# Kernel optimization log

Hardware: AMD Instinct MI355X
Metric: run time of the kernel (lower is better)

The kernel has to match this reference:

```python
import jax, jax.numpy as jnp
import numpy as np

E = 512   # embed_size
H = 8     # attn_heads
B = 4
S = 1024
EPS = 1e-5


def setup_inputs() -> dict:
    key = jax.random.key(0)
    ks = jax.random.split(key, 12)
    s_in = 1.0 / np.sqrt(E)
    s_cat = 1.0 / np.sqrt(H * E)
    s_ff = 1.0 / np.sqrt(4 * E)
    return {
        "x": jax.random.normal(ks[0], (B, S, E), jnp.float32),
        # projection weights stored [in, out] (transpose of torch Linear.weight)
        "Wq": jax.random.uniform(ks[1], (E, H * E), jnp.float32, -s_in, s_in),
        "Wk": jax.random.uniform(ks[2], (E, H * E), jnp.float32, -s_in, s_in),
        "Wv": jax.random.uniform(ks[3], (E, H * E), jnp.float32, -s_in, s_in),
        "Wo": jax.random.uniform(ks[4], (H * E, E), jnp.float32, -s_cat, s_cat),
        "g1": jnp.ones((E,), jnp.float32),
        "b1": jnp.zeros((E,), jnp.float32),
        "g2": jnp.ones((E,), jnp.float32),
        "b2": jnp.zeros((E,), jnp.float32),
        "W1": jax.random.uniform(ks[5], (E, 4 * E), jnp.float32, -s_in, s_in),
        "c1": jax.random.uniform(ks[6], (4 * E,), jnp.float32, -s_in, s_in),
        "W2": jax.random.uniform(ks[7], (4 * E, E), jnp.float32, -s_ff, s_ff),
        "c2": jax.random.uniform(ks[8], (E,), jnp.float32, -s_ff, s_ff),
    }


def _layernorm(x, g, b):
    mu = jnp.mean(x, axis=-1, keepdims=True)
    var = jnp.var(x, axis=-1, keepdims=True)
    return (x - mu) * jax.lax.rsqrt(var + EPS) * g + b


def reference(x, Wq, Wk, Wv, Wo, g1, b1, g2, b2, W1, c1, W2, c2):
    Bsz, Sl, Es = x.shape
    # project to [B, S, H, E] per-head (head dim == embed_size in this module)
    q = (x @ Wq).reshape(Bsz, Sl, H, Es)
    k = (x @ Wk).reshape(Bsz, Sl, H, Es)
    v = (x @ Wv).reshape(Bsz, Sl, H, Es)
    # scaled dot-product attention; note scale uses sqrt(embed_size)
    scores = jnp.einsum("bqhd,bkhd->bhqk", q, k) / jnp.sqrt(jnp.float32(Es))
    attn = jax.nn.softmax(scores, axis=-1)
    out = jnp.einsum("bhqk,bkhd->bqhd", attn, v).reshape(Bsz, Sl, H * Es)
    attn_scores = out @ Wo
    normed = _layernorm(attn_scores + x, g1, b1)
    h = jax.nn.relu(normed @ W1 + c1)
    ff = h @ W2 + c2
    return _layernorm(ff + normed, g2, b2)
```

## Files before the change

kernel.cpp:

```cpp
#include <hip/hip_runtime.h>
#include <hip/hip_fp8.h>

#define EBD   512
#define NHEAD 8
#define BSZ   4
#define SEQ   1024
#define MTOK  4096
#define HE    4096
#define FFD   2048

typedef __bf16 bf16;
typedef __attribute__((ext_vector_type(8))) __bf16 bf16x8;
typedef __attribute__((ext_vector_type(4))) float  f32x4;
typedef __attribute__((ext_vector_type(8))) int    i32x8;

__device__ __forceinline__ void async_load16(const void* g, void* l) {
  __builtin_amdgcn_global_load_lds(
      (const __attribute__((address_space(1))) void*)g,
      (__attribute__((address_space(3))) void*)l, 16, 0, 0);
}

#if __has_builtin(__builtin_amdgcn_cvt_pk_fp8_f32)
__device__ __forceinline__ int pk_fp8_lo(float a, float b, int old) {
  return __builtin_amdgcn_cvt_pk_fp8_f32(a, b, old, false);
}
__device__ __forceinline__ int pk_fp8_hi(float a, float b, int old) {
  return __builtin_amdgcn_cvt_pk_fp8_f32(a, b, old, true);
}
#else
__device__ __forceinline__ int pk_fp8_lo(float a, float b, int old) {
  __hip_fp8_e4m3 fa(a), fb(b);
  int w = (int)fa.__x | ((int)fb.__x << 8);
  return (old & ~0xffff) | w;
}
__device__ __forceinline__ int pk_fp8_hi(float a, float b, int old) {
  __hip_fp8_e4m3 fa(a), fb(b);
  int w = (int)fa.__x | ((int)fb.__x << 8);
  return (old & 0xffff) | (w << 16);
}
#endif

#if __has_builtin(__builtin_amdgcn_cvt_f32_fp8)
#define F8DEC(v, k) __builtin_amdgcn_cvt_f32_fp8((v), (k))
#else
__device__ __forceinline__ float __f8dec_sw(int v, int k) {
  __hip_fp8_e4m3 f; f.__x = (unsigned char)((v >> (8 * k)) & 0xff); return (float)f;
}
#define F8DEC(v, k) __f8dec_sw((v), (k))
#endif

__device__ __forceinline__ int4 pack16_fp8(const float* v) {
  int4 r;
  r.x = pk_fp8_hi(v[2],  v[3],  pk_fp8_lo(v[0],  v[1],  0));
  r.y = pk_fp8_hi(v[6],  v[7],  pk_fp8_lo(v[4],  v[5],  0));
  r.z = pk_fp8_hi(v[10], v[11], pk_fp8_lo(v[8],  v[9],  0));
  r.w = pk_fp8_hi(v[14], v[15], pk_fp8_lo(v[12], v[13], 0));
  return r;
}

__global__ void gemm_bt(const bf16* __restrict__ A, const bf16* __restrict__ Bt,
                        float* __restrict__ outF, bf16* __restrict__ outB,
                        const float* __restrict__ bias, const float* __restrict__ res,
                        int lda, int ldb, int ldc, int ldr, int K,
                        long long bAb, long long bAh, long long bBb, long long bBh,
                        long long bCb, long long bCh, int zdiv,
                        float scale, int relu)
{
  __shared__ __attribute__((aligned(16))) float Smem[4 * 2304];
  bf16* As = (bf16*)Smem;
  bf16* Bs = (bf16*)Smem + 128 * 64;

  const int t = threadIdx.x;
  const int w = t >> 6, l = t & 63;
  const int m0 = blockIdx.y * 128, n0 = blockIdx.x * 128;
  const int z = blockIdx.z;
  const int zb = z / zdiv, zh = z - zb * zdiv;

  const bf16* Ab = A + (size_t)zb * bAb + (size_t)zh * bAh;
  const bf16* Bb = Bt + (size_t)zb * bBb + (size_t)zh * bBh;

  const int srow = t >> 3;
  const int gch  = (((t & 7) ^ ((t >> 4) & 7))) * 8;
  const bf16* pA = Ab + (size_t)(m0 + srow) * lda + gch;
  const bf16* pB = Bb + (size_t)(n0 + srow) * ldb + gch;
  const size_t ldA32 = (size_t)32 * lda;
  const size_t ldB32 = (size_t)32 * ldb;

  bf16* ldsA = As + w * 512;
  bf16* ldsB = Bs + w * 512;

  const int wm = (w >> 1) * 64, wn = (w & 1) * 64;
  const int lr = l & 15;
  const int lc = l >> 4;

  f32x4 acc[4][4];
#pragma unroll
  for (int i = 0; i < 4; ++i)
#pragma unroll
    for (int j = 0; j < 4; ++j) { f32x4 zv = {0.f, 0.f, 0.f, 0.f}; acc[i][j] = zv; }

  const int nkt = K >> 6;
  for (int kt = 0; kt < nkt; ++kt) {
    __syncthreads();
#pragma unroll
    for (int j = 0; j < 4; ++j) {
      async_load16(pA + j * ldA32, ldsA + j * 2048);
      async_load16(pB + j * ldB32, ldsB + j * 2048);
    }
    pA += 64; pB += 64;
    __syncthreads();
#pragma unroll
    for (int ks = 0; ks < 2; ++ks) {
      bf16x8 af[4], bv[4];
#pragma unroll
      for (int i = 0; i < 4; ++i) {
        const int row = wm + i * 16 + lr;
        const int p = (ks * 4 + lc) ^ ((row >> 1) & 7);
        af[i] = *(const bf16x8*)&As[row * 64 + p * 8];
      }
#pragma unroll
      for (int i = 0; i < 4; ++i) {
        const int row = wn + i * 16 + lr;
        const int p = (ks * 4 + lc) ^ ((row >> 1) & 7);
        bv[i] = *(const bf16x8*)&Bs[row * 64 + p * 8];
      }
#pragma unroll
      for (int mi = 0; mi < 4; ++mi)
#pragma unroll
        for (int ni = 0; ni < 4; ++ni)
          acc[mi][ni] = __builtin_amdgcn_mfma_f32_16x16x32_bf16(af[mi], bv[ni], acc[mi][ni], 0, 0, 0);
    }
  }

  float* cs = Smem + w * 2304;
  const size_t offC = (size_t)zb * bCb + (size_t)zh * bCh;
  const int rq = (l >> 4) * 4;

#pragma unroll
  for (int p = 0; p < 2; ++p) {
    __syncthreads();
#pragma unroll
    for (int ni2 = 0; ni2 < 2; ++ni2) {
      const int ni = 2 * p + ni2;
      const int cl = ni2 * 16 + lr;
#pragma unroll
      for (int mi = 0; mi < 4; ++mi)
#pragma unroll
        for (int r = 0; r < 4; ++r)
          cs[(mi * 16 + rq + r) * 36 + cl] = acc[mi][ni][r];
    }
    __syncthreads();
    if (outB) {
      const int rl0 = l >> 2, c8 = (l & 3) * 8;
#pragma unroll
      for (int sub = 0; sub < 4; ++sub) {
        const int rl = sub * 16 + rl0;
        const int rowg = m0 + wm + rl;
        const int colg = n0 + wn + p * 32 + c8;
        float vv[8];
        *(f32x4*)&vv[0] = *(const f32x4*)&cs[rl * 36 + c8];
        *(f32x4*)&vv[4] = *(const f32x4*)&cs[rl * 36 + c8 + 4];
#pragma unroll
        for (int j = 0; j < 8; ++j) vv[j] *= scale;
        if (bias) {
          const float4 b0 = *(const float4*)(bias + colg);
          const float4 b1 = *(const float4*)(bias + colg + 4);
          vv[0] += b0.x; vv[1] += b0.y; vv[2] += b0.z; vv[3] += b0.w;
          vv[4] += b1.x; vv[5] += b1.y; vv[6] += b1.z; vv[7] += b1.w;
        }
        if (res) {
          const float4 r0 = *(const float4*)(res + (size_t)rowg * ldr + colg);
          const float4 r1 = *(const float4*)(res + (size_t)rowg * ldr + colg + 4);
          vv[0] += r0.x; vv[1] += r0.y; vv[2] += r0.z; vv[3] += r0.w;
          vv[4] += r1.x; vv[5] += r1.y; vv[6] += r1.z; vv[7] += r1.w;
        }
        if (relu)
#pragma unroll
          for (int j = 0; j < 8; ++j) vv[j] = fmaxf(vv[j], 0.0f);
        union { bf16 h8[8]; float4 f; } u;
#pragma unroll
        for (int j = 0; j < 8; ++j) u.h8[j] = (bf16)vv[j];
        *(float4*)(outB + offC + (size_t)rowg * ldc + colg) = u.f;
      }
    } else {
      const int rl0 = l >> 3, c4 = (l & 7) * 4;
#pragma unroll
      for (int sub = 0; sub < 8; ++sub) {
        const int rl = sub * 8 + rl0;
        const int rowg = m0 + wm + rl;
        const int colg = n0 + wn + p * 32 + c4;
        float4 v = *(const float4*)&cs[rl * 36 + c4];
        v.x *= scale; v.y *= scale; v.z *= scale; v.w *= scale;
        *(float4*)(outF + offC + (size_t)rowg * ldc + colg) = v;
      }
    }
  }
}

__global__ void gemm_f8(const unsigned char* __restrict__ A, const unsigned char* __restrict__ Bt,
                        float* __restrict__ outF, unsigned char* __restrict__ out8,
                        unsigned char* __restrict__ vTout, const float* __restrict__ rowdiv,
                        int lda, int ldb, int ldc, int K,
                        long long bAb, long long bAh, long long bBb, long long bBh,
                        long long bCb, long long bCh, int zdiv,
                        float scale, int mode, int vmode)
{
  __shared__ __attribute__((aligned(16))) float Smem[4 * 2304];
  unsigned char* As = (unsigned char*)Smem;
  unsigned char* Bs = As + 128 * 128;

  const int t = threadIdx.x;
  const int w = t >> 6, l = t & 63;
  const int m0 = blockIdx.y * 128, n0 = blockIdx.x * 128;
  const int z = blockIdx.z;
  const int zb = z / zdiv, zh = z - zb * zdiv;

  const unsigned char* Ab = A + (size_t)zb * bAb + (size_t)zh * bAh;
  const unsigned char* Bb = Bt + (size_t)zb * bBb + (size_t)zh * bBh;

  const int srow = t >> 3;
  const int gch  = ((t & 7) ^ ((t >> 4) & 7)) * 16;
  const unsigned char* pA = Ab + (size_t)(m0 + srow) * lda + gch;
  const unsigned char* pB = Bb + (size_t)(n0 + srow) * ldb + gch;
  const size_t ldA32 = (size_t)32 * lda;
  const size_t ldB32 = (size_t)32 * ldb;

  unsigned char* ldsA = As + w * 1024;
  unsigned char* ldsB = Bs + w * 1024;

  const int wm = (w >> 1) * 64, wn = (w & 1) * 64;
  const int lr = l & 15;
  const int lg = l >> 4;

  f32x4 acc[4][4];
#pragma unroll
  for (int i = 0; i < 4; ++i)
#pragma unroll
    for (int j = 0; j < 4; ++j) { f32x4 zv = {0.f, 0.f, 0.f, 0.f}; acc[i][j] = zv; }

  const int nkt = K >> 7;
  for (int kt = 0; kt < nkt; ++kt) {
    __syncthreads();
#pragma unroll
    for (int j = 0; j < 4; ++j) {
      async_load16(pA + j * ldA32, ldsA + j * 4096);
      async_load16(pB + j * ldB32, ldsB + j * 4096);
    }
    pA += 128; pB += 128;
    __syncthreads();
    i32x8 bv[4];
#pragma unroll
    for (int i = 0; i < 4; ++i) {
      const int row = wn + i * 16 + lr;
      const int s = (row >> 1) & 7;
      const int c0 = (2 * lg) ^ s, c1 = (2 * lg + 1) ^ s;
      const int4 lo = *(const int4*)&Bs[row * 128 + c0 * 16];
      const int4 hi = *(const int4*)&Bs[row * 128 + c1 * 16];
      i32x8 v = {lo.x, lo.y, lo.z, lo.w, hi.x, hi.y, hi.z, hi.w};
      bv[i] = v;
    }
#pragma unroll
    for (int mi = 0; mi < 4; ++mi) {
      const int row = wm + mi * 16 + lr;
      const int s = (row >> 1) & 7;
      const int c0 = (2 * lg) ^ s, c1 = (2 * lg + 1) ^ s;
      const int4 lo = *(const int4*)&As[row * 128 + c0 * 16];
      const int4 hi = *(const int4*)&As[row * 128 + c1 * 16];
      i32x8 af = {lo.x, lo.y, lo.z, lo.w, hi.x, hi.y, hi.z, hi.w};
#pragma unroll
      for (int ni = 0; ni < 4; ++ni)
        acc[mi][ni] = __builtin_amdgcn_mfma_scale_f32_16x16x128_f8f6f4(
            af, bv[ni], acc[mi][ni], 0, 0, 0, 0x7f7f7f7f, 0, 0x7f7f7f7f);
    }
  }

  float* cs = Smem + w * 2304;
  const size_t offC = (size_t)zb * bCb + (size_t)zh * bCh;
  const int rq = (l >> 4) * 4;

  if (vmode && n0 >= 8192) {
    const int b8 = (m0 + wm) >> 10;
    const int s0 = (m0 + wm) & 1023;
#pragma unroll
    for (int ph = 0; ph < 2; ++ph) {
      __syncthreads();
#pragma unroll
      for (int ni2 = 0; ni2 < 2; ++ni2) {
        const int ni = 2 * ph + ni2;
        const int cl = ni2 * 16 + lr;
#pragma unroll
        for (int mi = 0; mi < 4; ++mi)
#pragma unroll
          for (int r = 0; r < 4; ++r)
            cs[cl * 68 + mi * 16 + rq + r] = acc[mi][ni][r];
      }
      __syncthreads();
      const int c = l & 31, half = l >> 5;
      int e = (n0 - 8192) + wn + ph * 32 + c;
      const int h = e >> 9; e &= 511;
      unsigned char* dst = vTout + (((size_t)(b8 * 8 + h) * 512 + e) << 10) + s0 + half * 32;
      float vv[32];
#pragma unroll
      for (int j = 0; j < 8; ++j)
        *(f32x4*)&vv[4 * j] = *(const f32x4*)&cs[c * 68 + half * 32 + 4 * j];
#pragma unroll
      for (int j = 0; j < 32; ++j) vv[j] *= scale;
      *(int4*)dst        = pack16_fp8(&vv[0]);
      *(int4*)(dst + 16) = pack16_fp8(&vv[16]);
    }
    return;
  }

#pragma unroll
  for (int ph = 0; ph < 2; ++ph) {
    __syncthreads();
#pragma unroll
    for (int ni2 = 0; ni2 < 2; ++ni2) {
      const int ni = 2 * ph + ni2;
      const int cl = ni2 * 16 + lr;
#pragma unroll
      for (int mi = 0; mi < 4; ++mi)
#pragma unroll
        for (int r = 0; r < 4; ++r)
          cs[(mi * 16 + rq + r) * 36 + cl] = acc[mi][ni][r];
    }
    __syncthreads();
    if (mode == 3) {
      const int rl0 = l >> 3, c4 = (l & 7) * 4;
#pragma unroll
      for (int sub = 0; sub < 8; ++sub) {
        const int rl = sub * 8 + rl0;
        const int rowg = m0 + wm + rl;
        const int colg = n0 + wn + ph * 32 + c4;
        float4 v = *(const float4*)&cs[rl * 36 + c4];
        v.x *= scale; v.y *= scale; v.z *= scale; v.w *= scale;
        *(float4*)(outF + offC + (size_t)rowg * ldc + colg) = v;
      }
    } else {
      const int rl0 = l >> 1, c16 = (l & 1) * 16;
#pragma unroll
      for (int sub = 0; sub < 2; ++sub) {
        const int rl = sub * 32 + rl0;
        const int rowg = m0 + wm + rl;
        const int colg = n0 + wn + ph * 32 + c16;
        float vv[16];
#pragma unroll
        for (int j2 = 0; j2 < 4; ++j2)
          *(f32x4*)&vv[4 * j2] = *(const f32x4*)&cs[rl * 36 + c16 + 4 * j2];
        if (mode == 1) {
#pragma unroll
          for (int j = 0; j < 16; ++j) vv[j] = __expf(vv[j] * scale);
        } else if (mode == 2) {
          const float d = scale / rowdiv[(size_t)z * SEQ + rowg];
#pragma unroll
          for (int j = 0; j < 16; ++j) vv[j] *= d;
        } else {
#pragma unroll
          for (int j = 0; j < 16; ++j) vv[j] *= scale;
        }
        *(int4*)(out8 + offC + (size_t)rowg * ldc + colg) = pack16_fp8(vv);
      }
    }
  }
}

__global__ void cast_x_f8(const float* __restrict__ in, unsigned char* __restrict__ out, int n16) {
  int i = blockIdx.x * 256 + threadIdx.x;
  if (i >= n16) return;
  const float4* p = (const float4*)in + (size_t)i * 4;
  float vv[16];
  *(f32x4*)&vv[0]  = *(const f32x4*)&p[0];
  *(f32x4*)&vv[4]  = *(const f32x4*)&p[1];
  *(f32x4*)&vv[8]  = *(const f32x4*)&p[2];
  *(f32x4*)&vv[12] = *(const f32x4*)&p[3];
  ((int4*)out)[i] = pack16_fp8(vv);
}

struct WTList {
  const float* in[6];
  void* out[6];
  float scale[6];
  int isf8[6];
  int K[6], N[6];
  int start[7];
};
__global__ void transpose_cast_all(WTList L) {
  __shared__ float tile[32][33];
  int bid = blockIdx.x;
  int i = 0;
  while (bid >= L.start[i + 1]) ++i;
  int rel = bid - L.start[i];
  const int N = L.N[i], K = L.K[i];
  const int nx = N >> 5;
  const int n0 = (rel % nx) * 32, k0 = (rel / nx) * 32;
  const float* in = L.in[i];
  const float sc = L.scale[i];
  int tx = threadIdx.x, ty = threadIdx.y;
#pragma unroll
  for (int j = 0; j < 32; j += 8)
    tile[ty + j][tx] = in[(size_t)(k0 + ty + j) * N + n0 + tx];
  __syncthreads();
  if (L.isf8[i]) {
    unsigned char* out = (unsigned char*)L.out[i];
#pragma unroll
    for (int j = 0; j < 32; j += 8)
      out[(size_t)(n0 + ty + j) * K + k0 + tx] =
          (unsigned char)(pk_fp8_lo(tile[tx][ty + j] * sc, 0.f, 0) & 0xff);
  } else {
    bf16* out = (bf16*)L.out[i];
#pragma unroll
    for (int j = 0; j < 32; j += 8)
      out[(size_t)(n0 + ty + j) * K + k0 + tx] = (bf16)(tile[tx][ty + j] * sc);
  }
}

__global__ void rowsum_f8(const unsigned char* __restrict__ e, float* __restrict__ lsum) {
  int ln = threadIdx.x & 63, w = threadIdx.x >> 6;
  size_t row = (size_t)blockIdx.x * 4 + w;
  const int4 v = ((const int4*)(e + row * SEQ))[ln];
  float s = 0.0f;
  s += F8DEC(v.x, 0) + F8DEC(v.x, 1) + F8DEC(v.x, 2) + F8DEC(v.x, 3);
  s += F8DEC(v.y, 0) + F8DEC(v.y, 1) + F8DEC(v.y, 2) + F8DEC(v.y, 3);
  s += F8DEC(v.z, 0) + F8DEC(v.z, 1) + F8DEC(v.z, 2) + F8DEC(v.z, 3);
  s += F8DEC(v.w, 0) + F8DEC(v.w, 1) + F8DEC(v.w, 2) + F8DEC(v.w, 3);
#pragma unroll
  for (int d = 1; d < 64; d <<= 1) s += __shfl_xor(s, d);
  if (ln == 0) lsum[row] = s;
}

__global__ void reduce_ln(const float* __restrict__ parts, int ns,
                          const float* __restrict__ res, const float* __restrict__ bias,
                          const float* __restrict__ gw, const float* __restrict__ bw,
                          float* __restrict__ outF, bf16* __restrict__ outB) {
  int l = threadIdx.x & 63, w = threadIdx.x >> 6;
  int row = blockIdx.x * 4 + w;
  const long long pstr = (long long)MTOK * EBD;
  float4 a = {0.f, 0.f, 0.f, 0.f}, b = {0.f, 0.f, 0.f, 0.f};
  for (int s = 0; s < ns; ++s) {
    const float4* p = (const float4*)(parts + s * pstr + (size_t)row * EBD);
    float4 pa = p[l], pb = p[l + 64];
    a.x += pa.x; a.y += pa.y; a.z += pa.z; a.w += pa.w;
    b.x += pb.x; b.y += pb.y; b.z += pb.z; b.w += pb.w;
  }
  {
    const float4* p = (const float4*)(res + (size_t)row * EBD);
    float4 pa = p[l], pb = p[l + 64];
    a.x += pa.x; a.y += pa.y; a.z += pa.z; a.w += pa.w;
    b.x += pb.x; b.y += pb.y; b.z += pb.z; b.w += pb.w;
  }
  if (bias) {
    const float4* p = (const float4*)bias;
    float4 pa = p[l], pb = p[l + 64];
    a.x += pa.x; a.y += pa.y; a.z += pa.z; a.w += pa.w;
    b.x += pb.x; b.y += pb.y; b.z += pb.z; b.w += pb.w;
  }
  float s = a.x + a.y + a.z + a.w + b.x + b.y + b.z + b.w;
  float q = a.x * a.x + a.y * a.y + a.z * a.z + a.w * a.w
          + b.x * b.x + b.y * b.y + b.z * b.z + b.w * b.w;
#pragma unroll
  for (int d = 1; d < 64; d <<= 1) { s += __shfl_xor(s, d); q += __shfl_xor(q, d); }
  float mu = s * (1.0f / EBD);
  float var = q * (1.0f / EBD) - mu * mu;
  float rs = rsqrtf(var + 1e-5f);
  const float4* g4 = (const float4*)gw;
  const float4* b4 = (const float4*)bw;
  float4 ga = g4[l], gb = g4[l + 64], ba = b4[l], bb = b4[l + 64];
  float4 o0, o1;
  o0.x = (a.x - mu) * rs * ga.x + ba.x;
  o0.y = (a.y - mu) * rs * ga.y + ba.y;
  o0.z = (a.z - mu) * rs * ga.z + ba.z;
  o0.w = (a.w - mu) * rs * ga.w + ba.w;
  o1.x = (b.x - mu) * rs * gb.x + bb.x;
  o1.y = (b.y - mu) * rs * gb.y + bb.y;
  o1.z = (b.z - mu) * rs * gb.z + bb.z;
  o1.w = (b.w - mu) * rs * gb.w + bb.w;
  if (outF) {
    float4* q4 = (float4*)(outF + (size_t)row * EBD);
    q4[l] = o0; q4[l + 64] = o1;
  }
  if (outB) {
    union { bf16 h[4]; float2 f; } u0, u1;
    u0.h[0] = (bf16)o0.x; u0.h[1] = (bf16)o0.y; u0.h[2] = (bf16)o0.z; u0.h[3] = (bf16)o0.w;
    u1.h[0] = (bf16)o1.x; u1.h[1] = (bf16)o1.y; u1.h[2] = (bf16)o1.z; u1.h[3] = (bf16)o1.w;
    float2* r2 = (float2*)(outB + (size_t)row * EBD);
    r2[l] = u0.f; r2[l + 64] = u1.f;
  }
}

extern "C" void kernel_launch(void* const* d_in, const int* in_sizes, int n_in,
                              void* d_out, int out_size, void* d_ws, size_t ws_size,
                              hipStream_t stream) {
  const float* x  = (const float*)d_in[0];
  const float* Wq = (const float*)d_in[1];
  const float* Wk = (const float*)d_in[2];
  const float* Wv = (const float*)d_in[3];
  const float* Wo = (const float*)d_in[4];
  const float* g1 = (const float*)d_in[5];
  const float* b1 = (const float*)d_in[6];
  const float* g2 = (const float*)d_in[7];
  const float* b2 = (const float*)d_in[8];
  const float* W1 = (const float*)d_in[9];
  const float* c1 = (const float*)d_in[10];
  const float* W2 = (const float*)d_in[11];
  const float* c2 = (const float*)d_in[12];
  float* out = (float*)d_out;

  char* p = (char*)d_ws;
  auto take = [&](size_t bytes) { char* r = p; p += (bytes + 255) & ~(size_t)255; return r; };
  unsigned char* xb8    = (unsigned char*)take((size_t)MTOK * EBD);
  unsigned char* qk8    = (unsigned char*)take((size_t)MTOK * 2 * HE);
  unsigned char* vT8    = (unsigned char*)take((size_t)32 * EBD * SEQ);
  unsigned char* sc8    = (unsigned char*)take((size_t)32 * SEQ * SEQ);
  float*         lsum   = (float*)        take((size_t)32 * SEQ * 4);
  unsigned char* ao8    = (unsigned char*)take((size_t)MTOK * HE);
  float*         nF     = (float*)        take((size_t)MTOK * EBD * 4);
  bf16*          nB     = (bf16*)         take((size_t)MTOK * EBD * 2);
  bf16*          hb     = (bf16*)         take((size_t)MTOK * FFD * 2);
  unsigned char* Wqkv8T = (unsigned char*)take((size_t)3 * HE * EBD);
  unsigned char* Wo8T   = (unsigned char*)take((size_t)EBD * HE);
  bf16*          W1T    = (bf16*)         take((size_t)FFD * EBD * 2);
  bf16*          W2T    = (bf16*)         take((size_t)EBD * FFD * 2);
  float* parts = (float*)sc8;

  auto gemmf8 = [&](const unsigned char* A, const unsigned char* Bt, float* oF,
                    unsigned char* o8, unsigned char* vTo, const float* rdiv,
                    int Mm, int Nn, int Kk, int lda_, int ldb_, int ldc_,
                    long long bAb, long long bAh, long long bBb, long long bBh,
                    long long bCb, long long bCh, int zdiv_, int batch,
                    float sc_, int mode_, int vmode_) {
    dim3 g(Nn / 128, Mm / 128, batch);
    gemm_f8<<<g, dim3(256), 0, stream>>>(A, Bt, oF, o8, vTo, rdiv, lda_, ldb_, ldc_, Kk,
        bAb, bAh, bBb, bBh, bCb, bCh, zdiv_, sc_, mode_, vmode_);
  };
  auto gemmbf = [&](const bf16* A, const bf16* Bt, float* oF, bf16* oB,
                    const float* bias, const float* res,
                    int Mm, int Nn, int Kk, int lda_, int ldb_, int ldc_, int ldr_,
                    long long bAh, long long bBh, long long bCh, int batch,
                    float sc_, int relu_) {
    dim3 g(Nn / 128, Mm / 128, batch);
    gemm_bt<<<g, dim3(256), 0, stream>>>(A, Bt, oF, oB, bias, res,
        lda_, ldb_, ldc_, ldr_, Kk, 0, bAh, 0, bBh, 0, bCh, 64, sc_, relu_);
  };

  cast_x_f8<<<dim3(MTOK * EBD / 16 / 256), dim3(256), 0, stream>>>(x, xb8, MTOK * EBD / 16);
  {
    WTList L;
    const float* ins[6] = {Wq, Wk, Wv, Wo, W1, W2};
    void* outs[6] = {Wqkv8T, Wqkv8T + (size_t)HE * EBD, Wqkv8T + (size_t)2 * HE * EBD,
                     Wo8T, W1T, W2T};
    float scs[6] = {8.f, 8.f, 8.f, 16.f, 1.f, 1.f};
    int f8s[6] = {1, 1, 1, 1, 0, 0};
    int Ks[6] = {EBD, EBD, EBD, HE, EBD, FFD};
    int Ns[6] = {HE, HE, HE, EBD, FFD, EBD};
    int acc = 0;
    for (int i = 0; i < 6; ++i) {
      L.in[i] = ins[i]; L.out[i] = outs[i]; L.scale[i] = scs[i]; L.isf8[i] = f8s[i];
      L.K[i] = Ks[i]; L.N[i] = Ns[i]; L.start[i] = acc;
      acc += (Ks[i] / 32) * (Ns[i] / 32);
    }
    L.start[6] = acc;
    transpose_cast_all<<<dim3(acc), dim3(32, 8), 0, stream>>>(L);
  }

  gemmf8(xb8, Wqkv8T, nullptr, qk8, vT8, nullptr, MTOK, 3 * HE, EBD,
         EBD, EBD, 2 * HE, 0, 0, 0, 0, 0, 0, 64, 1, 0.125f, 0, 1);

  const float qs = 0.04419417382415922f;
  gemmf8(qk8, qk8 + HE, nullptr, sc8, nullptr, nullptr, SEQ, SEQ, EBD,
         2 * HE, 2 * HE, SEQ,
         (long long)SEQ * 2 * HE, EBD, (long long)SEQ * 2 * HE, EBD,
         (long long)8 * SEQ * SEQ, (long long)SEQ * SEQ, 8, 32, qs, 1, 0);

  rowsum_f8<<<dim3(32 * SEQ / 4), dim3(256), 0, stream>>>(sc8, lsum);

  gemmf8(sc8, vT8, nullptr, ao8, nullptr, lsum, SEQ, EBD, SEQ,
         SEQ, SEQ, HE,
         (long long)8 * SEQ * SEQ, (long long)SEQ * SEQ,
         (long long)8 * EBD * SEQ, (long long)EBD * SEQ,
         (long long)SEQ * HE, (long long)EBD, 8, 32, 16.0f, 2, 0);

  gemmf8(ao8, Wo8T, parts, nullptr, nullptr, nullptr, MTOK, EBD, 1024,
         HE, HE, EBD, 0, 1024, 0, 1024, 0, (long long)MTOK * EBD, 64, 4,
         1.0f / 256.0f, 3, 0);
  reduce_ln<<<dim3(MTOK / 4), dim3(256), 0, stream>>>(parts, 4, x, nullptr, g1, b1, nF, nB);

  gemmbf(nB, W1T, nullptr, hb, c1, nullptr, MTOK, FFD, EBD,
         EBD, EBD, FFD, 0, 0, 0, 0, 1, 1.0f, 1);
  gemmbf(hb, W2T, parts, nullptr, nullptr, nullptr, MTOK, EBD, 512,
         FFD, FFD, EBD, 0, 512, 512, (long long)MTOK * EBD, 4, 1.0f, 0);
  reduce_ln<<<dim3(MTOK / 4), dim3(256), 0, stream>>>(parts, 4, nF, c2, g2, b2, out, nullptr);
}
```

Measured before the change: 296.9 us.

## Move FFN GEMMs to FP8 and fuse softmax row sums into score GEMM

The two feed-forward GEMMs now use the FP8 GEMM kernel instead of the bf16 one. W1 and W2 are pre-scaled and cast to FP8, and the LayerNorm output and hidden activations are stored as FP8, with bias and ReLU moved into the FP8 epilogue. The separate rowsum kernel is dropped: the score GEMM accumulates exp row sums with atomics into lsum, which cast_x_f8 zeroes in one extra block. This removes a kernel launch, a full reread of the score matrix, and bf16 traffic and MFMA cost in the FFN, in exchange for lower FFN precision and float atomics whose summation order is nondeterministic.

After: 278.9 us. 6.1% less time.

```diff
diff --git a/kernel.cpp b/kernel.cpp
--- a/kernel.cpp
+++ b/kernel.cpp
@@ -10,7 +10,6 @@
 #define FFD   2048
 
 typedef __bf16 bf16;
-typedef __attribute__((ext_vector_type(8))) __bf16 bf16x8;
 typedef __attribute__((ext_vector_type(4))) float  f32x4;
 typedef __attribute__((ext_vector_type(8))) int    i32x8;
 
@@ -38,15 +37,6 @@
   int w = (int)fa.__x | ((int)fb.__x << 8);
   return (old & 0xffff) | (w << 16);
 }
-#endif
-
-#if __has_builtin(__builtin_amdgcn_cvt_f32_fp8)
-#define F8DEC(v, k) __builtin_amdgcn_cvt_f32_fp8((v), (k))
-#else
-__device__ __forceinline__ float __f8dec_sw(int v, int k) {
-  __hip_fp8_e4m3 f; f.__x = (unsigned char)((v >> (8 * k)) & 0xff); return (float)f;
-}
-#define F8DEC(v, k) __f8dec_sw((v), (k))
 #endif
 
 __device__ __forceinline__ int4 pack16_fp8(const float* v) {
@@ -58,152 +48,14 @@
   return r;
 }
 
-__global__ void gemm_bt(const bf16* __restrict__ A, const bf16* __restrict__ Bt,
-                        float* __restrict__ outF, bf16* __restrict__ outB,
-                        const float* __restrict__ bias, const float* __restrict__ res,
-                        int lda, int ldb, int ldc, int ldr, int K,
-                        long long bAb, long long bAh, long long bBb, long long bBh,
-                        long long bCb, long long bCh, int zdiv,
-                        float scale, int relu)
-{
-  __shared__ __attribute__((aligned(16))) float Smem[4 * 2304];
-  bf16* As = (bf16*)Smem;
-  bf16* Bs = (bf16*)Smem + 128 * 64;
-
-  const int t = threadIdx.x;
-  const int w = t >> 6, l = t & 63;
-  const int m0 = blockIdx.y * 128, n0 = blockIdx.x * 128;
-  const int z = blockIdx.z;
-  const int zb = z / zdiv, zh = z - zb * zdiv;
-
-  const bf16* Ab = A + (size_t)zb * bAb + (size_t)zh * bAh;
-  const bf16* Bb = Bt + (size_t)zb * bBb + (size_t)zh * bBh;
-
-  const int srow = t >> 3;
-  const int gch  = (((t & 7) ^ ((t >> 4) & 7))) * 8;
-  const bf16* pA = Ab + (size_t)(m0 + srow) * lda + gch;
-  const bf16* pB = Bb + (size_t)(n0 + srow) * ldb + gch;
-  const size_t ldA32 = (size_t)32 * lda;
-  const size_t ldB32 = (size_t)32 * ldb;
-
-  bf16* ldsA = As + w * 512;
-  bf16* ldsB = Bs + w * 512;
-
-  const int wm = (w >> 1) * 64, wn = (w & 1) * 64;
-  const int lr = l & 15;
-  const int lc = l >> 4;
-
-  f32x4 acc[4][4];
-#pragma unroll
-  for (int i = 0; i < 4; ++i)
-#pragma unroll
-    for (int j = 0; j < 4; ++j) { f32x4 zv = {0.f, 0.f, 0.f, 0.f}; acc[i][j] = zv; }
-
-  const int nkt = K >> 6;
-  for (int kt = 0; kt < nkt; ++kt) {
-    __syncthreads();
-#pragma unroll
-    for (int j = 0; j < 4; ++j) {
-      async_load16(pA + j * ldA32, ldsA + j * 2048);
-      async_load16(pB + j * ldB32, ldsB + j * 2048);
-    }
-    pA += 64; pB += 64;
-    __syncthreads();
-#pragma unroll
-    for (int ks = 0; ks < 2; ++ks) {
-      bf16x8 af[4], bv[4];
-#pragma unroll
-      for (int i = 0; i < 4; ++i) {
-        const int row = wm + i * 16 + lr;
-        const int p = (ks * 4 + lc) ^ ((row >> 1) & 7);
-        af[i] = *(const bf16x8*)&As[row * 64 + p * 8];
-      }
-#pragma unroll
-      for (int i = 0; i < 4; ++i) {
-        const int row = wn + i * 16 + lr;
-        const int p = (ks * 4 + lc) ^ ((row >> 1) & 7);
-        bv[i] = *(const bf16x8*)&Bs[row * 64 + p * 8];
-      }
-#pragma unroll
-      for (int mi = 0; mi < 4; ++mi)
-#pragma unroll
-        for (int ni = 0; ni < 4; ++ni)
-          acc[mi][ni] = __builtin_amdgcn_mfma_f32_16x16x32_bf16(af[mi], bv[ni], acc[mi][ni], 0, 0, 0);
-    }
-  }
-
-  float* cs = Smem + w * 2304;
-  const size_t offC = (size_t)zb * bCb + (size_t)zh * bCh;
-  const int rq = (l >> 4) * 4;
-
-#pragma unroll
-  for (int p = 0; p < 2; ++p) {
-    __syncthreads();
-#pragma unroll
-    for (int ni2 = 0; ni2 < 2; ++ni2) {
-      const int ni = 2 * p + ni2;
-      const int cl = ni2 * 16 + lr;
-#pragma unroll
-      for (int mi = 0; mi < 4; ++mi)
-#pragma unroll
-        for (int r = 0; r < 4; ++r)
-          cs[(mi * 16 + rq + r) * 36 + cl] = acc[mi][ni][r];
-    }
-    __syncthreads();
-    if (outB) {
-      const int rl0 = l >> 2, c8 = (l & 3) * 8;
-#pragma unroll
-      for (int sub = 0; sub < 4; ++sub) {
-        const int rl = sub * 16 + rl0;
-        const int rowg = m0 + wm + rl;
-        const int colg = n0 + wn + p * 32 + c8;
-        float vv[8];
-        *(f32x4*)&vv[0] = *(const f32x4*)&cs[rl * 36 + c8];
-        *(f32x4*)&vv[4] = *(const f32x4*)&cs[rl * 36 + c8 + 4];
-#pragma unroll
-        for (int j = 0; j < 8; ++j) vv[j] *= scale;
-        if (bias) {
-          const float4 b0 = *(const float4*)(bias + colg);
-          const float4 b1 = *(const float4*)(bias + colg + 4);
-          vv[0] += b0.x; vv[1] += b0.y; vv[2] += b0.z; vv[3] += b0.w;
-          vv[4] += b1.x; vv[5] += b1.y; vv[6] += b1.z; vv[7] += b1.w;
-        }
-        if (res) {
-          const float4 r0 = *(const float4*)(res + (size_t)rowg * ldr + colg);
-          const float4 r1 = *(const float4*)(res + (size_t)rowg * ldr + colg + 4);
-          vv[0] += r0.x; vv[1] += r0.y; vv[2] += r0.z; vv[3] += r0.w;
-          vv[4] += r1.x; vv[5] += r1.y; vv[6] += r1.z; vv[7] += r1.w;
-        }
-        if (relu)
-#pragma unroll
-          for (int j = 0; j < 8; ++j) vv[j] = fmaxf(vv[j], 0.0f);
-        union { bf16 h8[8]; float4 f; } u;
-#pragma unroll
-        for (int j = 0; j < 8; ++j) u.h8[j] = (bf16)vv[j];
-        *(float4*)(outB + offC + (size_t)rowg * ldc + colg) = u.f;
-      }
-    } else {
-      const int rl0 = l >> 3, c4 = (l & 7) * 4;
-#pragma unroll
-      for (int sub = 0; sub < 8; ++sub) {
-        const int rl = sub * 8 + rl0;
-        const int rowg = m0 + wm + rl;
-        const int colg = n0 + wn + p * 32 + c4;
-        float4 v = *(const float4*)&cs[rl * 36 + c4];
-        v.x *= scale; v.y *= scale; v.z *= scale; v.w *= scale;
-        *(float4*)(outF + offC + (size_t)rowg * ldc + colg) = v;
-      }
-    }
-  }
-}
-
 __global__ void gemm_f8(const unsigned char* __restrict__ A, const unsigned char* __restrict__ Bt,
                         float* __restrict__ outF, unsigned char* __restrict__ out8,
                         unsigned char* __restrict__ vTout, const float* __restrict__ rowdiv,
+                        const float* __restrict__ bias, float* __restrict__ lsum,
                         int lda, int ldb, int ldc, int K,
                         long long bAb, long long bAh, long long bBb, long long bBh,
                         long long bCb, long long bCh, int zdiv,
-                        float scale, int mode, int vmode)
+                        float scale, int mode, int relu, int vmode)
 {
   __shared__ __attribute__((aligned(16))) float Smem[4 * 2304];
   unsigned char* As = (unsigned char*)Smem;
@@ -311,6 +163,9 @@
     return;
   }
 
+  const int rl0 = l >> 1, c16 = (l & 1) * 16;
+  float rsum[2] = {0.f, 0.f};
+
 #pragma unroll
   for (int ph = 0; ph < 2; ++ph) {
     __syncthreads();
@@ -326,10 +181,10 @@
     }
     __syncthreads();
     if (mode == 3) {
-      const int rl0 = l >> 3, c4 = (l & 7) * 4;
+      const int prl0 = l >> 3, c4 = (l & 7) * 4;
 #pragma unroll
       for (int sub = 0; sub < 8; ++sub) {
-        const int rl = sub * 8 + rl0;
+        const int rl = sub * 8 + prl0;
         const int rowg = m0 + wm + rl;
         const int colg = n0 + wn + ph * 32 + c4;
         float4 v = *(const float4*)&cs[rl * 36 + c4];
@@ -337,7 +192,6 @@
         *(float4*)(outF + offC + (size_t)rowg * ldc + colg) = v;
       }
     } else {
-      const int rl0 = l >> 1, c16 = (l & 1) * 16;
 #pragma unroll
       for (int sub = 0; sub < 2; ++sub) {
         const int rl = sub * 32 + rl0;
@@ -347,26 +201,57 @@
 #pragma unroll
         for (int j2 = 0; j2 < 4; ++j2)
           *(f32x4*)&vv[4 * j2] = *(const f32x4*)&cs[rl * 36 + c16 + 4 * j2];
+#pragma unroll
+        for (int j = 0; j < 16; ++j) vv[j] *= scale;
+        if (bias) {
+#pragma unroll
+          for (int j2 = 0; j2 < 4; ++j2) {
+            const float4 b0 = *(const float4*)(bias + colg + 4 * j2);
+            vv[4 * j2] += b0.x; vv[4 * j2 + 1] += b0.y;
+            vv[4 * j2 + 2] += b0.z; vv[4 * j2 + 3] += b0.w;
+          }
+        }
+        if (relu)
+#pragma unroll
+          for (int j = 0; j < 16; ++j) vv[j] = fmaxf(vv[j], 0.0f);
         if (mode == 1) {
-#pragma unroll
-          for (int j = 0; j < 16; ++j) vv[j] = __expf(vv[j] * scale);
+          float s = 0.0f;
+#pragma unroll
+          for (int j = 0; j < 16; ++j) { vv[j] = __expf(vv[j]); s += vv[j]; }
+          rsum[sub] += s;
         } else if (mode == 2) {
-          const float d = scale / rowdiv[(size_t)z * SEQ + rowg];
+          const float d = 1.0f / rowdiv[(size_t)z * SEQ + rowg];
 #pragma unroll
           for (int j = 0; j < 16; ++j) vv[j] *= d;
-        } else {
-#pragma unroll
-          for (int j = 0; j < 16; ++j) vv[j] *= scale;
         }
         *(int4*)(out8 + offC + (size_t)rowg * ldc + colg) = pack16_fp8(vv);
       }
     }
   }
-}
-
-__global__ void cast_x_f8(const float* __restrict__ in, unsigned char* __restrict__ out, int n16) {
+  if (mode == 1 && lsum) {
+#pragma unroll
+    for (int sub = 0; sub < 2; ++sub) {
+      float s = rsum[sub] + __shfl_xor(rsum[sub], 1);
+      if (!(l & 1)) {
+        const int rowg = m0 + wm + sub * 32 + rl0;
+        atomicAdd(&lsum[(size_t)z * SEQ + rowg], s);
+      }
+    }
+  }
+}
+
+__global__ void cast_x_f8(const float* __restrict__ in, unsigned char* __restrict__ out,
+                          int n16, float* __restrict__ lsum) {
   int i = blockIdx.x * 256 + threadIdx.x;
-  if (i >= n16) return;
+  if (i >= n16) {
+    if (blockIdx.x == (unsigned)(n16 / 256)) {
+      float4 zv = {0.f, 0.f, 0.f, 0.f};
+      float4* q = (float4*)lsum;
+#pragma unroll
+      for (int j = 0; j < 32; ++j) q[threadIdx.x * 32 + j] = zv;
+    }
+    return;
+  }
   const float4* p = (const float4*)in + (size_t)i * 4;
   float vv[16];
   *(f32x4*)&vv[0]  = *(const f32x4*)&p[0];
@@ -378,9 +263,8 @@
 
 struct WTList {
   const float* in[6];
-  void* out[6];
+  unsigned char* out[6];
   float scale[6];
-  int isf8[6];
   int K[6], N[6];
   int start[7];
 };
@@ -395,43 +279,22 @@
   const int n0 = (rel % nx) * 32, k0 = (rel / nx) * 32;
   const float* in = L.in[i];
   const float sc = L.scale[i];
+  unsigned char* out = L.out[i];
   int tx = threadIdx.x, ty = threadIdx.y;
 #pragma unroll
   for (int j = 0; j < 32; j += 8)
     tile[ty + j][tx] = in[(size_t)(k0 + ty + j) * N + n0 + tx];
   __syncthreads();
-  if (L.isf8[i]) {
-    unsigned char* out = (unsigned char*)L.out[i];
-#pragma unroll
-    for (int j = 0; j < 32; j += 8)
-      out[(size_t)(n0 + ty + j) * K + k0 + tx] =
-          (unsigned char)(pk_fp8_lo(tile[tx][ty + j] * sc, 0.f, 0) & 0xff);
-  } else {
-    bf16* out = (bf16*)L.out[i];
-#pragma unroll
-    for (int j = 0; j < 32; j += 8)
-      out[(size_t)(n0 + ty + j) * K + k0 + tx] = (bf16)(tile[tx][ty + j] * sc);
-  }
-}
-
-__global__ void rowsum_f8(const unsigned char* __restrict__ e, float* __restrict__ lsum) {
-  int ln = threadIdx.x & 63, w = threadIdx.x >> 6;
-  size_t row = (size_t)blockIdx.x * 4 + w;
-  const int4 v = ((const int4*)(e + row * SEQ))[ln];
-  float s = 0.0f;
-  s += F8DEC(v.x, 0) + F8DEC(v.x, 1) + F8DEC(v.x, 2) + F8DEC(v.x, 3);
-  s += F8DEC(v.y, 0) + F8DEC(v.y, 1) + F8DEC(v.y, 2) + F8DEC(v.y, 3);
-  s += F8DEC(v.z, 0) + F8DEC(v.z, 1) + F8DEC(v.z, 2) + F8DEC(v.z, 3);
-  s += F8DEC(v.w, 0) + F8DEC(v.w, 1) + F8DEC(v.w, 2) + F8DEC(v.w, 3);
-#pragma unroll
-  for (int d = 1; d < 64; d <<= 1) s += __shfl_xor(s, d);
-  if (ln == 0) lsum[row] = s;
+#pragma unroll
+  for (int j = 0; j < 32; j += 8)
+    out[(size_t)(n0 + ty + j) * K + k0 + tx] =
+        (unsigned char)(pk_fp8_lo(tile[tx][ty + j] * sc, 0.f, 0) & 0xff);
 }
 
 __global__ void reduce_ln(const float* __restrict__ parts, int ns,
                           const float* __restrict__ res, const float* __restrict__ bias,
                           const float* __restrict__ gw, const float* __restrict__ bw,
-                          float* __restrict__ outF, bf16* __restrict__ outB) {
+                          float* __restrict__ outF, unsigned char* __restrict__ out8) {
   int l = threadIdx.x & 63, w = threadIdx.x >> 6;
   int row = blockIdx.x * 4 + w;
   const long long pstr = (long long)MTOK * EBD;
@@ -478,12 +341,10 @@
     float4* q4 = (float4*)(outF + (size_t)row * EBD);
     q4[l] = o0; q4[l + 64] = o1;
   }
-  if (outB) {
-    union { bf16 h[4]; float2 f; } u0, u1;
-    u0.h[0] = (bf16)o0.x; u0.h[1] = (bf16)o0.y; u0.h[2] = (bf16)o0.z; u0.h[3] = (bf16)o0.w;
-    u1.h[0] = (bf16)o1.x; u1.h[1] = (bf16)o1.y; u1.h[2] = (bf16)o1.z; u1.h[3] = (bf16)o1.w;
-    float2* r2 = (float2*)(outB + (size_t)row * EBD);
-    r2[l] = u0.f; r2[l + 64] = u1.f;
+  if (out8) {
+    int* o = (int*)(out8 + (size_t)row * EBD);
+    o[l]      = pk_fp8_hi(o0.z, o0.w, pk_fp8_lo(o0.x, o0.y, 0));
+    o[l + 64] = pk_fp8_hi(o1.z, o1.w, pk_fp8_lo(o1.x, o1.y, 0));
   }
 }
 
@@ -514,47 +375,39 @@
   float*         lsum   = (float*)        take((size_t)32 * SEQ * 4);
   unsigned char* ao8    = (unsigned char*)take((size_t)MTOK * HE);
   float*         nF     = (float*)        take((size_t)MTOK * EBD * 4);
-  bf16*          nB     = (bf16*)         take((size_t)MTOK * EBD * 2);
-  bf16*          hb     = (bf16*)         take((size_t)MTOK * FFD * 2);
+  unsigned char* n8     = (unsigned char*)take((size_t)MTOK * EBD);
+  unsigned char* h8     = (unsigned char*)take((size_t)MTOK * FFD);
   unsigned char* Wqkv8T = (unsigned char*)take((size_t)3 * HE * EBD);
   unsigned char* Wo8T   = (unsigned char*)take((size_t)EBD * HE);
-  bf16*          W1T    = (bf16*)         take((size_t)FFD * EBD * 2);
-  bf16*          W2T    = (bf16*)         take((size_t)EBD * FFD * 2);
+  unsigned char* W18T   = (unsigned char*)take((size_t)FFD * EBD);
+  unsigned char* W28T   = (unsigned char*)take((size_t)EBD * FFD);
   float* parts = (float*)sc8;
 
   auto gemmf8 = [&](const unsigned char* A, const unsigned char* Bt, float* oF,
                     unsigned char* o8, unsigned char* vTo, const float* rdiv,
+                    const float* bias_, float* lsum_,
                     int Mm, int Nn, int Kk, int lda_, int ldb_, int ldc_,
                     long long bAb, long long bAh, long long bBb, long long bBh,
                     long long bCb, long long bCh, int zdiv_, int batch,
-                    float sc_, int mode_, int vmode_) {
+                    float sc_, int mode_, int relu_, int vmode_) {
     dim3 g(Nn / 128, Mm / 128, batch);
-    gemm_f8<<<g, dim3(256), 0, stream>>>(A, Bt, oF, o8, vTo, rdiv, lda_, ldb_, ldc_, Kk,
-        bAb, bAh, bBb, bBh, bCb, bCh, zdiv_, sc_, mode_, vmode_);
+    gemm_f8<<<g, dim3(256), 0, stream>>>(A, Bt, oF, o8, vTo, rdiv, bias_, lsum_,
+        lda_, ldb_, ldc_, Kk, bAb, bAh, bBb, bBh, bCb, bCh, zdiv_, sc_, mode_, relu_, vmode_);
   };
-  auto gemmbf = [&](const bf16* A, const bf16* Bt, float* oF, bf16* oB,
-                    const float* bias, const float* res,
-                    int Mm, int Nn, int Kk, int lda_, int ldb_, int ldc_, int ldr_,
-                    long long bAh, long long bBh, long long bCh, int batch,
-                    float sc_, int relu_) {
-    dim3 g(Nn / 128, Mm / 128, batch);
-    gemm_bt<<<g, dim3(256), 0, stream>>>(A, Bt, oF, oB, bias, res,
-        lda_, ldb_, ldc_, ldr_, Kk, 0, bAh, 0, bBh, 0, bCh, 64, sc_, relu_);
-  };
-
-  cast_x_f8<<<dim3(MTOK * EBD / 16 / 256), dim3(256), 0, stream>>>(x, xb8, MTOK * EBD / 16);
+
+  cast_x_f8<<<dim3(MTOK * EBD / 16 / 256 + 1), dim3(256), 0, stream>>>(
+      x, xb8, MTOK * EBD / 16, lsum);
   {
     WTList L;
     const float* ins[6] = {Wq, Wk, Wv, Wo, W1, W2};
-    void* outs[6] = {Wqkv8T, Wqkv8T + (size_t)HE * EBD, Wqkv8T + (size_t)2 * HE * EBD,
-                     Wo8T, W1T, W2T};
-    float scs[6] = {8.f, 8.f, 8.f, 16.f, 1.f, 1.f};
-    int f8s[6] = {1, 1, 1, 1, 0, 0};
+    unsigned char* outs[6] = {Wqkv8T, Wqkv8T + (size_t)HE * EBD, Wqkv8T + (size_t)2 * HE * EBD,
+                              Wo8T, W18T, W28T};
+    float scs[6] = {8.f, 8.f, 8.f, 16.f, 8.f, 16.f};
     int Ks[6] = {EBD, EBD, EBD, HE, EBD, FFD};
     int Ns[6] = {HE, HE, HE, EBD, FFD, EBD};
     int acc = 0;
     for (int i = 0; i < 6; ++i) {
-      L.in[i] = ins[i]; L.out[i] = outs[i]; L.scale[i] = scs[i]; L.isf8[i] = f8s[i];
+      L.in[i] = ins[i]; L.out[i] = outs[i]; L.scale[i] = scs[i];
       L.K[i] = Ks[i]; L.N[i] = Ns[i]; L.start[i] = acc;
       acc += (Ks[i] / 32) * (Ns[i] / 32);
     }
@@ -562,31 +415,33 @@
     transpose_cast_all<<<dim3(acc), dim3(32, 8), 0, stream>>>(L);
   }
 
-  gemmf8(xb8, Wqkv8T, nullptr, qk8, vT8, nullptr, MTOK, 3 * HE, EBD,
-         EBD, EBD, 2 * HE, 0, 0, 0, 0, 0, 0, 64, 1, 0.125f, 0, 1);
+  gemmf8(xb8, Wqkv8T, nullptr, qk8, vT8, nullptr, nullptr, nullptr,
+         MTOK, 3 * HE, EBD, EBD, EBD, 2 * HE,
+         0, 0, 0, 0, 0, 0, 64, 1, 0.125f, 0, 0, 1);
 
   const float qs = 0.04419417382415922f;
-  gemmf8(qk8, qk8 + HE, nullptr, sc8, nullptr, nullptr, SEQ, SEQ, EBD,
-         2 * HE, 2 * HE, SEQ,
+  gemmf8(qk8, qk8 + HE, nullptr, sc8, nullptr, nullptr, nullptr, lsum,
+         SEQ, SEQ, EBD, 2 * HE, 2 * HE, SEQ,
          (long long)SEQ * 2 * HE, EBD, (long long)SEQ * 2 * HE, EBD,
-         (long long)8 * SEQ * SEQ, (long long)SEQ * SEQ, 8, 32, qs, 1, 0);
-
-  rowsum_f8<<<dim3(32 * SEQ / 4), dim3(256), 0, stream>>>(sc8, lsum);
-
-  gemmf8(sc8, vT8, nullptr, ao8, nullptr, lsum, SEQ, EBD, SEQ,
-         SEQ, SEQ, HE,
+         (long long)8 * SEQ * SEQ, (long long)SEQ * SEQ, 8, 32, qs, 1, 0, 0);
+
+  gemmf8(sc8, vT8, nullptr, ao8, nullptr, lsum, nullptr, nullptr,
+         SEQ, EBD, SEQ, SEQ, SEQ, HE,
          (long long)8 * SEQ * SEQ, (long long)SEQ * SEQ,
          (long long)8 * EBD * SEQ, (long long)EBD * SEQ,
-         (long long)SEQ * HE, (long long)EBD, 8, 32, 16.0f, 2, 0);
-
-  gemmf8(ao8, Wo8T, parts, nullptr, nullptr, nullptr, MTOK, EBD, 1024,
-         HE, HE, EBD, 0, 1024, 0, 1024, 0, (long long)MTOK * EBD, 64, 4,
-         1.0f / 256.0f, 3, 0);
-  reduce_ln<<<dim3(MTOK / 4), dim3(256), 0, stream>>>(parts, 4, x, nullptr, g1, b1, nF, nB);
-
-  gemmbf(nB, W1T, nullptr, hb, c1, nullptr, MTOK, FFD, EBD,
-         EBD, EBD, FFD, 0, 0, 0, 0, 1, 1.0f, 1);
-  gemmbf(hb, W2T, parts, nullptr, nullptr, nullptr, MTOK, EBD, 512,
-         FFD, FFD, EBD, 0, 512, 512, (long long)MTOK * EBD, 4, 1.0f, 0);
+         (long long)SEQ * HE, (long long)EBD, 8, 32, 16.0f, 2, 0, 0);
+
+  gemmf8(ao8, Wo8T, parts, nullptr, nullptr, nullptr, nullptr, nullptr,
+         MTOK, EBD, 1024, HE, HE, EBD,
+         0, 1024, 0, 1024, 0, (long long)MTOK * EBD, 64, 4, 1.0f / 256.0f, 3, 0, 0);
+  reduce_ln<<<dim3(MTOK / 4), dim3(256), 0, stream>>>(parts, 4, x, nullptr, g1, b1, nF, n8);
+
+  gemmf8(n8, W18T, nullptr, h8, nullptr, nullptr, c1, nullptr,
+         MTOK, FFD, EBD, EBD, EBD, FFD,
+         0, 0, 0, 0, 0, 0, 64, 1, 0.125f, 0, 1, 0);
+
+  gemmf8(h8, W28T, parts, nullptr, nullptr, nullptr, nullptr, nullptr,
+         MTOK, EBD, 512, FFD, FFD, EBD,
+         0, 512, 0, 512, 0, (long long)MTOK * EBD, 64, 4, 1.0f / 16.0f, 3, 0, 0);
   reduce_ln<<<dim3(MTOK / 4), dim3(256), 0, stream>>>(parts, 4, nF, c2, g2, b2, out, nullptr);
 }
```
